# Kernel optimization log

Measured on AMD Instinct MI355X. Metric: run time of the kernel, lower is better.

Reference implementation:

```python
import jax, jax.numpy as jnp
import numpy as np

B, S, D, H, CD, TV, BS = 64, 128, 1024, 16, 128, 512, 4
HD = D // H          # head dim 64
MLP = 4 * D


def _ln(x, w):
    # SEDD-style LayerNorm: no bias, learned scale only
    m = x.mean(-1, keepdims=True)
    v = jnp.var(x, axis=-1, keepdims=True)
    return (x - m) * jax.lax.rsqrt(v + 1e-5) * w


def _rope(q, cos, sin):
    # q: (B, S, H, hd); cos/sin: (S, hd) with cat(freqs, freqs) layout
    h = HD // 2
    rot = jnp.concatenate([-q[..., h:], q[..., :h]], axis=-1)
    return q * cos[None, :, None, :] + rot * sin[None, :, None, :]


def _attn(q, k, v, mask):
    # q,k,v: (B, H, Lq/Lk, hd); mask broadcastable to (B, H, Lq, Lk), True = attend
    s = jnp.einsum('bhqd,bhkd->bhqk', q, k) / jnp.sqrt(jnp.asarray(HD, q.dtype))
    s = jnp.where(mask, s, jnp.asarray(-1e30, s.dtype))
    p = jax.nn.softmax(s, axis=-1)
    return jnp.einsum('bhqk,bhkd->bhqd', p, v)


def setup_inputs() -> dict:
    key = jax.random.key(0)
    ks = jax.random.split(key, 16)
    f = lambda k, shp, sc: jax.random.normal(k, shp, jnp.float32) * sc
    inp = {}
    inp['x'] = f(ks[0], (B, 2 * S, D), 1.0)
    inp['c'] = f(ks[1], (B, CD), 1.0)
    inp['encoder_out'] = f(ks[2], (B, TV, D), 1.0)
    enc_mask = np.ones((B, TV), dtype=bool)
    enc_mask[:, TV * 3 // 4:] = False
    inp['encoder_mask'] = jnp.asarray(enc_mask)
    # block diffusion training mask, (2S, 2S): M_BD | M_OBC | M_BC
    idx = np.arange(2 * S)
    q_idx, kv_idx = idx[:, None], idx[None, :]
    x0_q, x0_kv = q_idx >= S, kv_idx >= S
    bq = np.where(x0_q, (q_idx - S) // BS, q_idx // BS)
    bkv = np.where(x0_kv, (kv_idx - S) // BS, kv_idx // BS)
    m = ((bq == bkv) & (x0_q == x0_kv)) | ((bq > bkv) & x0_kv & (~x0_q)) | ((bq >= bkv) & x0_kv & x0_q)
    inp['mask'] = jnp.asarray(m)
    # rotary cos/sin for length S (applied identically to both halves)
    inv = 1.0 / (10000.0 ** (np.arange(0, HD, 2, dtype=np.float64) / HD))
    fr = np.einsum('i,j->ij', np.arange(S), inv)
    emb = np.concatenate([fr, fr], axis=-1)
    inp['cos'] = jnp.asarray(np.cos(emb), jnp.float32)
    inp['sin'] = jnp.asarray(np.sin(emb), jnp.float32)
    sc = 1.0 / np.sqrt(D)
    inp['norm1_w'] = jnp.ones((D,), jnp.float32)
    inp['w_qkv'] = f(ks[3], (D, 3 * D), sc)
    inp['w_attn_out'] = f(ks[4], (D, D), sc)
    inp['adaLN_w'] = f(ks[5], (CD, 6 * D), 0.02)  # nonzero so gates are active
    inp['adaLN_b'] = f(ks[6], (6 * D,), 0.02)
    inp['ca_norm_w'] = jnp.ones((D,), jnp.float32)
    inp['w_q'] = f(ks[7], (D, D), sc)
    inp['w_kv'] = f(ks[8], (D, 2 * D), sc)
    inp['w_o'] = f(ks[9], (D, D), sc)
    inp['norm2_w'] = jnp.ones((D,), jnp.float32)
    inp['w_mlp1'] = f(ks[10], (D, MLP), sc)
    inp['b_mlp1'] = jnp.zeros((MLP,), jnp.float32)
    inp['w_mlp2'] = f(ks[11], (MLP, D), 1.0 / np.sqrt(MLP))
    inp['b_mlp2'] = jnp.zeros((D,), jnp.float32)
    return inp


def reference(x, c, encoder_out, encoder_mask, mask, cos, sin,
              norm1_w, w_qkv, w_attn_out, adaLN_w, adaLN_b,
              ca_norm_w, w_q, w_kv, w_o, norm2_w,
              w_mlp1, b_mlp1, w_mlp2, b_mlp2):
    mod = (c @ adaLN_w + adaLN_b)[:, None, :]
    sh_msa, sc_msa, g_msa, sh_mlp, sc_mlp, g_mlp = jnp.split(mod, 6, axis=-1)
    x_skip = x
    xn = _ln(x, norm1_w) * (1.0 + sc_msa) + sh_msa  # modulate

    def get_qkv(xh):  # xh: (B, S, D) -> rotated q, k and v, each (B, S, H, hd)
        qkv = (xh @ w_qkv).reshape(B, S, 3, H, HD)
        return _rope(qkv[:, :, 0], cos, sin), _rope(qkv[:, :, 1], cos, sin), qkv[:, :, 2]

    q1, k1, v1 = get_qkv(xn[:, :S])
    q2, k2, v2 = get_qkv(xn[:, S:])
    q = jnp.concatenate([q1, q2], 1).transpose(0, 2, 1, 3)  # (B, H, 2S, hd)
    k = jnp.concatenate([k1, k2], 1).transpose(0, 2, 1, 3)
    v = jnp.concatenate([v1, v2], 1).transpose(0, 2, 1, 3)
    a = _attn(q, k, v, mask[None, None]).transpose(0, 2, 1, 3).reshape(B, 2 * S, D)
    x = x_skip + g_msa * (a @ w_attn_out)  # bias_dropout_add_scale (inference)

    # cross-attention to visual features
    r = x
    xc = _ln(x, ca_norm_w)
    qc = (xc @ w_q).reshape(B, 2 * S, H, HD).transpose(0, 2, 1, 3)
    kvc = (encoder_out @ w_kv).reshape(B, TV, 2, H, HD)
    kc = kvc[:, :, 0].transpose(0, 2, 1, 3)
    vc = kvc[:, :, 1].transpose(0, 2, 1, 3)
    ac = _attn(qc, kc, vc, encoder_mask[:, None, None, :]).transpose(0, 2, 1, 3).reshape(B, 2 * S, D)
    x = r + ac @ w_o

    # adaLN-modulated MLP (gelu-tanh)
    h = _ln(x, norm2_w) * (1.0 + sc_mlp) + sh_mlp
    m = jax.nn.gelu(h @ w_mlp1 + b_mlp1, approximate=True) @ w_mlp2 + b_mlp2
    return x + g_mlp * m
```

## Files before the change

### kernel.cpp

```cpp
#include <hip/hip_runtime.h>
#include <hip/hip_bf16.h>
#include <math.h>

typedef __hip_bfloat16 bf16;
typedef __attribute__((ext_vector_type(8))) short bf16x8;
typedef __attribute__((ext_vector_type(4))) float f32x4;

#define B_   64
#define S_   128
#define L_   256
#define D_   1024
#define H_   16
#define HD_  64
#define CD_  128
#define TV_  512
#define MLP_ 4096
#define SIXD (6*D_)
#define GB   16
#define NG   (B_/GB)
#define MG   (GB*L_)

__device__ __forceinline__ float b2f(bf16 v){ return __bfloat162float(v); }
__device__ __forceinline__ bf16  f2b(float v){ return __float2bfloat16(v); }
__device__ __forceinline__ unsigned short f2bu(float v){
    bf16 b = __float2bfloat16(v);
    unsigned short u; __builtin_memcpy(&u, &b, 2); return u;
}
__device__ __forceinline__ short f2bs(float v){ return (short)f2bu(v); }
__device__ __forceinline__ float ldf(const void* p, size_t i, bool f32){
    return f32 ? ((const float*)p)[i] : b2f(((const bf16*)p)[i]);
}
__device__ __forceinline__ void gload16(const void* g, void* l){
    __builtin_amdgcn_global_load_lds(
        (const __attribute__((address_space(1))) void*)g,
        (__attribute__((address_space(3))) void*)l, 16, 0, 0);
}

__global__ void detect_kernel(const unsigned short* __restrict__ x, int* __restrict__ flag)
{
    __shared__ int cnt;
    if (threadIdx.x == 0) cnt = 0;
    __syncthreads();
    int local = 0;
    for (int i = threadIdx.x; i < 1024; i += 256) {
        unsigned short h = x[2*i];
        int e = (h >> 7) & 0xff;
        if (e >= 117 && e <= 133) local++;
    }
    atomicAdd(&cnt, local);
    __syncthreads();
    if (threadIdx.x == 0) flag[0] = (cnt < 512) ? 1 : 0;
}

#define BM 64
#define BN 64
#define BK 16
__global__ __launch_bounds__(256) void gemm_kernel(
    const int* __restrict__ dt, int opmask,
    const void* __restrict__ A, size_t aOff,
    const void* __restrict__ W,
    int M, int N, int K,
    const void* __restrict__ bias, int act,
    const float* __restrict__ mod, int gate_off, int row0,
    const void* __restrict__ resb,
    bf16* __restrict__ outb, float* __restrict__ outf)
{
    const bool f32 = dt[0] != 0;
    const bool aF = f32 && (opmask & 1);
    const bool rF = f32 && (opmask & 2);
    const bool wF = f32;

    __shared__ float As[BK][BM+1];
    __shared__ float Ws[BK][BN+1];
    int tid = threadIdx.x;
    int bm = blockIdx.y * BM;
    int bn = blockIdx.x * BN;
    int ty = tid >> 4, tx = tid & 15;
    float acc[4][4];
#pragma unroll
    for (int i=0;i<4;i++)
#pragma unroll
        for (int j=0;j<4;j++) acc[i][j]=0.f;

    for (int k0=0; k0<K; k0+=BK) {
#pragma unroll
        for (int i=0;i<4;i++) {
            int idx = tid + i*256;
            int m = idx >> 4, k = idx & 15;
            As[k][m] = ldf(A, aOff + (size_t)(bm+m)*K + k0 + k, aF);
        }
#pragma unroll
        for (int i=0;i<4;i++) {
            int idx = tid + i*256;
            int k = idx >> 6, n = idx & 63;
            Ws[k][n] = ldf(W, (size_t)(k0+k)*N + bn + n, wF);
        }
        __syncthreads();
#pragma unroll
        for (int k=0;k<BK;k++) {
            float a0[4], w0[4];
#pragma unroll
            for (int i=0;i<4;i++) a0[i] = As[k][ty*4+i];
#pragma unroll
            for (int j=0;j<4;j++) w0[j] = Ws[k][tx*4+j];
#pragma unroll
            for (int i=0;i<4;i++)
#pragma unroll
                for (int j=0;j<4;j++)
                    acc[i][j] += a0[i]*w0[j];
        }
        __syncthreads();
    }

#pragma unroll
    for (int i=0;i<4;i++) {
        int m = bm + ty*4 + i;
#pragma unroll
        for (int j=0;j<4;j++) {
            int n = bn + tx*4 + j;
            float v = acc[i][j];
            if (bias) v += ldf(bias, n, wF);
            if (act==1) {
                float x3 = v*v*v;
                v = 0.5f*v*(1.f + tanhf(0.7978845608028654f*(v + 0.044715f*x3)));
            }
            if (mod)  v *= mod[(size_t)((row0+m)>>8)*SIXD + gate_off + n];
            size_t o = (size_t)m*N + n;
            if (resb) v += ldf(resb, o, rF);
            if (outf) outf[o] = v;
            else      outb[o] = f2b(v);
        }
    }
}

__global__ __launch_bounds__(256) void transpose_w_kernel(
    const int* __restrict__ dt, const void* __restrict__ W,
    bf16* __restrict__ Wt, int K, int N)
{
    const bool f32 = dt[0] != 0;
    __shared__ float t[32][33];
    int n0 = blockIdx.x * 32, k0 = blockIdx.y * 32;
    int tx = threadIdx.x & 31, ty = threadIdx.x >> 5;
#pragma unroll
    for (int r = 0; r < 4; ++r)
        t[ty + r*8][tx] = ldf(W, (size_t)(k0 + ty + r*8)*N + n0 + tx, f32);
    __syncthreads();
#pragma unroll
    for (int r = 0; r < 4; ++r)
        Wt[(size_t)(n0 + ty + r*8)*K + k0 + tx] = f2b(t[tx][ty + r*8]);
}

__global__ __launch_bounds__(256) void mfma_gemm(
    const int* __restrict__ dt, int aDin,
    const void* __restrict__ A, size_t aOff,
    const bf16* __restrict__ Wt,
    int M, int N, int K,
    const void* __restrict__ bias, int act,
    const float* __restrict__ mod, int gate_off, int row0,
    const void* __restrict__ resb, int rDin,
    bf16* __restrict__ outb, float* __restrict__ outf)
{
    const bool f32 = dt[0] != 0;
    const bool aF = f32 && aDin;
    const bool rF = f32 && rDin;
    (void)M;

    __shared__ __align__(16) short As[128*40];
    __shared__ __align__(16) short Bs[128*32];

    int tid  = threadIdx.x;
    int lane = tid & 63, wid = tid >> 6;
    int wr = wid >> 1, wc = wid & 1;
    size_t bm = (size_t)blockIdx.y * 128;
    size_t bn = (size_t)blockIdx.x * 128;

    f32x4 acc[4][4];
#pragma unroll
    for (int i=0;i<4;i++)
#pragma unroll
        for (int j=0;j<4;j++) acc[i][j] = (f32x4){0.f,0.f,0.f,0.f};

    const int rr  = lane & 15;
    const int ksg = (lane >> 4) * 8;

    const short* Ab = (const short*)A + aOff;
    const float* Af = (const float*)A + aOff;
    const short* Wts = (const short*)Wt;

    if (!aF) {
        for (int k0 = 0; k0 < K; k0 += 32) {
#pragma unroll
            for (int c = 0; c < 2; ++c) {
                int u = wid*128 + c*64 + lane;
                gload16(Ab  + (bm + (u>>2))*K + k0 + (u&3)*8, As + (wid*128 + c*64)*8);
                gload16(Wts + (bn + (u>>2))*K + k0 + (u&3)*8, Bs + (wid*128 + c*64)*8);
            }
            __syncthreads();
            bf16x8 av[4], bv[4];
#pragma unroll
            for (int i=0;i<4;i++) av[i] = *(const bf16x8*)(As + (wr*64 + i*16 + rr)*32 + ksg);
#pragma unroll
            for (int j=0;j<4;j++) bv[j] = *(const bf16x8*)(Bs + (wc*64 + j*16 + rr)*32 + ksg);
#pragma unroll
            for (int i=0;i<4;i++)
#pragma unroll
                for (int j=0;j<4;j++)
                    acc[i][j] = __builtin_amdgcn_mfma_f32_16x16x32_bf16(av[i], bv[j], acc[i][j], 0, 0, 0);
            __syncthreads();
        }
    } else {
        const int r0 = tid >> 2,         p0 = tid & 3;
        const int r1 = (tid + 256) >> 2, p1 = (tid + 256) & 3;
        for (int k0 = 0; k0 < K; k0 += 32) {
            const float* s0 = Af + (bm+r0)*K + k0 + p0*8;
            float4 u0 = *(const float4*)s0;
            float4 u1 = *(const float4*)(s0+4);
            bf16x8 t0;
            t0[0]=f2bs(u0.x); t0[1]=f2bs(u0.y); t0[2]=f2bs(u0.z); t0[3]=f2bs(u0.w);
            t0[4]=f2bs(u1.x); t0[5]=f2bs(u1.y); t0[6]=f2bs(u1.z); t0[7]=f2bs(u1.w);
            *(bf16x8*)(As + r0*40 + p0*8) = t0;
            const float* s1 = Af + (bm+r1)*K + k0 + p1*8;
            float4 u2 = *(const float4*)s1;
            float4 u3 = *(const float4*)(s1+4);
            bf16x8 t1;
            t1[0]=f2bs(u2.x); t1[1]=f2bs(u2.y); t1[2]=f2bs(u2.z); t1[3]=f2bs(u2.w);
            t1[4]=f2bs(u3.x); t1[5]=f2bs(u3.y); t1[6]=f2bs(u3.z); t1[7]=f2bs(u3.w);
            *(bf16x8*)(As + r1*40 + p1*8) = t1;
#pragma unroll
            for (int c = 0; c < 2; ++c) {
                int u = wid*128 + c*64 + lane;
                gload16(Wts + (bn + (u>>2))*K + k0 + (u&3)*8, Bs + (wid*128 + c*64)*8);
            }
            __syncthreads();
            bf16x8 av[4], bv[4];
#pragma unroll
            for (int i=0;i<4;i++) av[i] = *(const bf16x8*)(As + (wr*64 + i*16 + rr)*40 + ksg);
#pragma unroll
            for (int j=0;j<4;j++) bv[j] = *(const bf16x8*)(Bs + (wc*64 + j*16 + rr)*32 + ksg);
#pragma unroll
            for (int i=0;i<4;i++)
#pragma unroll
                for (int j=0;j<4;j++)
                    acc[i][j] = __builtin_amdgcn_mfma_f32_16x16x32_bf16(av[i], bv[j], acc[i][j], 0, 0, 0);
            __syncthreads();
        }
    }

    const int cc = lane & 15;
    const int rb = (lane >> 4) * 4;
#pragma unroll
    for (int j=0;j<4;j++) {
        int gcol = (int)bn + wc*64 + j*16 + cc;
        float bvadd = bias ? ldf(bias, gcol, f32) : 0.f;
#pragma unroll
        for (int i=0;i<4;i++) {
#pragma unroll
            for (int r2=0;r2<4;r2++) {
                int grow = (int)bm + wr*64 + i*16 + rb + r2;
                float v = acc[i][j][r2] + bvadd;
                if (act == 1) {
                    float x3 = v*v*v;
                    v = 0.5f*v*(1.f + tanhf(0.7978845608028654f*(v + 0.044715f*x3)));
                }
                if (mod) v *= mod[(size_t)((row0+grow)>>8)*SIXD + gate_off + gcol];
                size_t o = (size_t)grow*N + gcol;
                if (resb) v += ldf(resb, o, rF);
                if (outf) outf[o] = v;
                else      outb[o] = f2b(v);
            }
        }
    }
}

__global__ __launch_bounds__(256) void ln_kernel(
    const int* __restrict__ dt, int x_din,
    const void* __restrict__ xb, const void* __restrict__ w,
    const float* __restrict__ mod, int sh_off, int sc_off,
    bf16* __restrict__ out)
{
    const bool f32 = dt[0] != 0;
    const bool xF = f32 && x_din;
    const bool wF = f32;
    int row = blockIdx.x;
    int b   = row >> 8;
    int tid = threadIdx.x;
    float xv[4];
    float s=0.f, s2=0.f;
#pragma unroll
    for (int i=0;i<4;i++) {
        int d = tid + i*256;
        float v = ldf(xb, (size_t)row*D_ + d, xF);
        xv[i]=v; s+=v; s2+=v*v;
    }
    __shared__ float r1[256], r2[256];
    r1[tid]=s; r2[tid]=s2; __syncthreads();
    for (int off=128; off>0; off>>=1) {
        if (tid<off){ r1[tid]+=r1[tid+off]; r2[tid]+=r2[tid+off]; }
        __syncthreads();
    }
    float mean = r1[0]*(1.f/D_);
    float var  = r2[0]*(1.f/D_) - mean*mean;
    float rstd = rsqrtf(var + 1e-5f);
#pragma unroll
    for (int i=0;i<4;i++) {
        int d = tid + i*256;
        float y = (xv[i]-mean)*rstd*ldf(w, d, wF);
        if (mod) y = y*(1.f + mod[(size_t)b*SIXD + sc_off + d])
                     + mod[(size_t)b*SIXD + sh_off + d];
        out[(size_t)row*D_ + d] = f2b(y);
    }
}

__global__ __launch_bounds__(256) void rope_kernel(
    const int* __restrict__ dt, bf16* __restrict__ qkv,
    const void* __restrict__ cosb, const void* __restrict__ sinb)
{
    const bool f32 = dt[0] != 0;
    int g  = blockIdx.x*256 + threadIdx.x;
    int d  = g & 31;
    int h  = (g>>5) & 15;
    int qk = (g>>9) & 1;
    int t  = (g>>10) & 255;
    int b  = g >> 18;
    int pos = t & (S_-1);
    bf16* p = qkv + ((size_t)(b*L_+t)*3 + qk)*D_ + h*HD_;
    float c0 = ldf(cosb, pos*HD_ + d,    f32), sn0 = ldf(sinb, pos*HD_ + d,    f32);
    float c1 = ldf(cosb, pos*HD_ + d+32, f32), sn1 = ldf(sinb, pos*HD_ + d+32, f32);
    float lo = b2f(p[d]), hi = b2f(p[d+32]);
    p[d]    = f2b(lo*c0 - hi*sn0);
    p[d+32] = f2b(hi*c1 + lo*sn1);
}

template<int MODE>
__global__ __launch_bounds__(256) void attn_mfma_kernel(
    const bf16* __restrict__ qsrc, const bf16* __restrict__ kvsrc,
    bf16* __restrict__ out)
{
    constexpr int NT = MODE ? 12 : 8;
    int blk  = blockIdx.x;
    int half = blk & 1;
    int h    = (blk >> 1) & 15;
    int b    = blk >> 5;
    int tid  = threadIdx.x, lane = tid & 63, w = tid >> 6;
    int g = lane >> 4, c = lane & 15;

    __shared__ __align__(16) short Kt[2][32][72];
    __shared__ __align__(16) short Vt[2][64][40];
    __shared__ __align__(16) short Pl[4][32][40];

    const size_t krstride = MODE ? 2048 : 3072;
    const bf16* Kbase = MODE ? kvsrc + ((size_t)b*512*2    )*1024 + h*64
                             : kvsrc + ((size_t)b*256*3 + 1)*1024 + h*64;
    const bf16* Vbase = MODE ? kvsrc + ((size_t)b*512*2 + 1)*1024 + h*64
                             : kvsrc + ((size_t)b*256*3 + 2)*1024 + h*64;
    const size_t qstride = MODE ? 1024 : 3072;
    const bf16* Qbase = MODE ? qsrc + (size_t)b*256*1024 + h*64
                             : qsrc + (size_t)b*256*3*1024 + h*64;

    bf16x8 qf[2][2];
#pragma unroll
    for (int qb=0; qb<2; ++qb) {
        int qi = half*128 + w*32 + qb*16 + c;
#pragma unroll
        for (int dc=0; dc<2; ++dc)
            qf[qb][dc] = *(const bf16x8*)(Qbase + (size_t)qi*qstride + dc*32 + g*8);
    }

    f32x4 oacc[2][4];
    float mrow[2][4], lrow[2][4];
#pragma unroll
    for (int qb=0; qb<2; ++qb){
#pragma unroll
        for (int dl=0; dl<4; ++dl) oacc[qb][dl] = (f32x4){0.f,0.f,0.f,0.f};
#pragma unroll
        for (int r=0; r<4; ++r){ mrow[qb][r] = -1e30f; lrow[qb][r] = 0.f; }
    }

    auto stage = [&](int kt, int buf){
        for (int u = tid; u < 512; u += 256) {
            int k = u >> 4, d8 = (u & 15)*4;
            *(uint2*)&Kt[buf][k][d8] =
                *(const uint2*)(Kbase + (size_t)(kt*32+k)*krstride + d8);
        }
        for (int u = tid; u < 512; u += 256) {
            int k = u >> 4, d4 = (u & 15)*4;
            uint2 vv = *(const uint2*)(Vbase + (size_t)(kt*32+k)*krstride + d4);
            short* vp = (short*)&vv;
#pragma unroll
            for (int j=0;j<4;++j) Vt[buf][d4+j][k] = vp[j];
        }
    };

    stage(0, 0);
    __syncthreads();

    for (int kt = 0; kt < NT; ++kt) {
        int buf = kt & 1;
        if (kt+1 < NT) stage(kt+1, buf^1);

        bool need = MODE ? true : ((half==0 && kt==w) || (kt>=4 && (kt-4)<=w));
        if (need) {
            bf16x8 kf[2][2], vf[4];
#pragma unroll
            for (int kc=0;kc<2;++kc)
#pragma unroll
                for (int dc=0;dc<2;++dc)
                    kf[kc][dc] = *(const bf16x8*)&Kt[buf][kc*16 + c][dc*32 + g*8];
#pragma unroll
            for (int dl=0;dl<4;++dl)
                vf[dl] = *(const bf16x8*)&Vt[buf][dl*16 + c][g*8];

#pragma unroll
            for (int qb=0;qb<2;++qb) {
                f32x4 s0 = (f32x4){0.f,0.f,0.f,0.f};
                f32x4 s1 = (f32x4){0.f,0.f,0.f,0.f};
                s0 = __builtin_amdgcn_mfma_f32_16x16x32_bf16(qf[qb][0], kf[0][0], s0, 0,0,0);
                s0 = __builtin_amdgcn_mfma_f32_16x16x32_bf16(qf[qb][1], kf[0][1], s0, 0,0,0);
                s1 = __builtin_amdgcn_mfma_f32_16x16x32_bf16(qf[qb][0], kf[1][0], s1, 0,0,0);
                s1 = __builtin_amdgcn_mfma_f32_16x16x32_bf16(qf[qb][1], kf[1][1], s1, 0,0,0);

                bool v0 = true, v1 = true;
                if (MODE == 0) {
                    int bq  = w*8 + qb*4 + g;
                    int ki0 = kt*32 + c, ki1 = ki0 + 16;
                    bool xk0 = ki0 >= 128, xk1 = ki1 >= 128;
                    int bk0 = (ki0 & 127) >> 2, bk1 = (ki1 & 127) >> 2;
                    v0 = xk0 ? (half ? (bq >= bk0) : (bq > bk0)) : (!half && bq == bk0);
                    v1 = xk1 ? (half ? (bq >= bk1) : (bq > bk1)) : (!half && bq == bk1);
                }
                float a0[4], a1[4];
#pragma unroll
                for (int r=0;r<4;++r){
                    a0[r] = v0 ? s0[r]*0.125f : -1e30f;
                    a1[r] = v1 ? s1[r]*0.125f : -1e30f;
                }
                float p0[4], p1[4];
#pragma unroll
                for (int r=0;r<4;++r){
                    float t = fmaxf(a0[r], a1[r]);
                    t = fmaxf(t, __shfl_xor(t,1));
                    t = fmaxf(t, __shfl_xor(t,2));
                    t = fmaxf(t, __shfl_xor(t,4));
                    t = fmaxf(t, __shfl_xor(t,8));
                    float mn = fmaxf(mrow[qb][r], t);
                    float scale = __expf(mrow[qb][r] - mn);
                    mrow[qb][r] = mn;
                    p0[r] = __expf(a0[r] - mn);
                    p1[r] = __expf(a1[r] - mn);
                    float rs = p0[r] + p1[r];
                    rs += __shfl_xor(rs,1);
                    rs += __shfl_xor(rs,2);
                    rs += __shfl_xor(rs,4);
                    rs += __shfl_xor(rs,8);
                    lrow[qb][r] = lrow[qb][r]*scale + rs;
#pragma unroll
                    for (int dl=0;dl<4;++dl) oacc[qb][dl][r] *= scale;
                }
#pragma unroll
                for (int r=0;r<4;++r){
                    Pl[w][qb*16 + g*4 + r][c]      = f2bs(p0[r]);
                    Pl[w][qb*16 + g*4 + r][16 + c] = f2bs(p1[r]);
                }
            }
            asm volatile("s_waitcnt lgkmcnt(0)" ::: "memory");
            __builtin_amdgcn_sched_barrier(0);
#pragma unroll
            for (int qb=0;qb<2;++qb) {
                bf16x8 pa = *(const bf16x8*)&Pl[w][qb*16 + c][g*8];
#pragma unroll
                for (int dl=0;dl<4;++dl)
                    oacc[qb][dl] = __builtin_amdgcn_mfma_f32_16x16x32_bf16(pa, vf[dl], oacc[qb][dl], 0,0,0);
            }
        }
        __syncthreads();
    }

#pragma unroll
    for (int qb=0;qb<2;++qb){
#pragma unroll
        for (int r=0;r<4;++r){
            float inv = 1.f / lrow[qb][r];
            int qi = half*128 + w*32 + qb*16 + g*4 + r;
            bf16* op = out + (size_t)(b*256 + qi)*1024 + h*64;
#pragma unroll
            for (int dl=0;dl<4;++dl)
                op[dl*16 + c] = f2b(oacc[qb][dl][r] * inv);
        }
    }
}

extern "C" void kernel_launch(void* const* d_in, const int* in_sizes, int n_in,
                              void* d_out, int out_size, void* d_ws, size_t ws_size,
                              hipStream_t stream)
{
    (void)in_sizes; (void)n_in; (void)out_size; (void)ws_size;
    const void* x    = d_in[0];
    const void* c    = d_in[1];
    const void* enc  = d_in[2];
    const void* cosb = d_in[5];
    const void* sinb = d_in[6];
    const void* n1w  = d_in[7];
    const void* wqkv = d_in[8];
    const void* wao  = d_in[9];
    const void* adw  = d_in[10];
    const void* adb  = d_in[11];
    const void* cnw  = d_in[12];
    const void* wq   = d_in[13];
    const void* wkv  = d_in[14];
    const void* wo   = d_in[15];
    const void* n2w  = d_in[16];
    const void* wm1  = d_in[17];
    const void* bm1  = d_in[18];
    const void* wm2  = d_in[19];
    const void* bm2  = d_in[20];
    float* fout = (float*)d_out;

    char* p = (char*)d_ws;
    int*   dt  = (int*)p;    p += 256;
    float* mod = (float*)p;  p += (size_t)B_*SIXD*4;
    bf16*  A   = (bf16*)p;   p += (size_t)B_*L_*D_*2;
    bf16*  C   = (bf16*)p;   p += (size_t)B_*L_*D_*2;
    bf16*  Dch = (bf16*)p;   p += (size_t)GB*TV_*2*D_*2;
    bf16*  Wt1 = (bf16*)p;   p += (size_t)D_*MLP_*2;
    bf16*  Wt2 = (bf16*)p;   p += (size_t)D_*MLP_*2;
    bf16*  Bq  = (bf16*)d_out;

    const int M = B_*L_;
    dim3 blk(256);

    detect_kernel<<<1, blk, 0, stream>>>((const unsigned short*)x, dt);
    gemm_kernel<<<dim3(SIXD/BN, B_/BM), blk, 0, stream>>>(
        dt, 1, c, 0, adw, B_, SIXD, CD_, adb, 0, nullptr, 0, 0, nullptr, nullptr, mod);
    ln_kernel<<<M, blk, 0, stream>>>(dt, 1, x, n1w, mod, 0*D_, 1*D_, A);
    transpose_w_kernel<<<dim3(3*D_/32, D_/32), blk, 0, stream>>>(dt, wqkv, Wt1, D_, 3*D_);
    for (int g=0; g<NG; g++) {
        mfma_gemm<<<dim3(3*D_/128, MG/128), blk, 0, stream>>>(
            dt, 0, A, (size_t)g*MG*D_, Wt1, MG, 3*D_, D_,
            nullptr, 0, nullptr, 0, 0, nullptr, 0, Dch, nullptr);
        rope_kernel<<<(GB*L_*2*H_*32)/256, blk, 0, stream>>>(dt, Dch, cosb, sinb);
        attn_mfma_kernel<0><<<GB*H_*2, blk, 0, stream>>>(Dch, Dch, Bq + (size_t)g*MG*D_);
    }
    transpose_w_kernel<<<dim3(D_/32, D_/32), blk, 0, stream>>>(dt, wao, Wt1, D_, D_);
    mfma_gemm<<<dim3(D_/128, M/128), blk, 0, stream>>>(
        dt, 0, Bq, 0, Wt1, M, D_, D_,
        nullptr, 0, mod, 2*D_, 0, x, 1, C, nullptr);
    ln_kernel<<<M, blk, 0, stream>>>(dt, 0, C, cnw, nullptr, 0, 0, A);
    transpose_w_kernel<<<dim3(D_/32, D_/32), blk, 0, stream>>>(dt, wq, Wt1, D_, D_);
    mfma_gemm<<<dim3(D_/128, M/128), blk, 0, stream>>>(
        dt, 0, A, 0, Wt1, M, D_, D_,
        nullptr, 0, nullptr, 0, 0, nullptr, 0, Bq, nullptr);
    transpose_w_kernel<<<dim3(2*D_/32, D_/32), blk, 0, stream>>>(dt, wkv, Wt1, D_, 2*D_);
    for (int g=0; g<NG; g++) {
        mfma_gemm<<<dim3(2*D_/128, (GB*TV_)/128), blk, 0, stream>>>(
            dt, 1, enc, (size_t)g*GB*TV_*D_, Wt1, GB*TV_, 2*D_, D_,
            nullptr, 0, nullptr, 0, 0, nullptr, 0, Dch, nullptr);
        attn_mfma_kernel<1><<<GB*H_*2, blk, 0, stream>>>(
            Bq + (size_t)g*MG*D_, Dch, A + (size_t)g*MG*D_);
    }
    transpose_w_kernel<<<dim3(D_/32, D_/32), blk, 0, stream>>>(dt, wo, Wt1, D_, D_);
    mfma_gemm<<<dim3(D_/128, M/128), blk, 0, stream>>>(
        dt, 0, A, 0, Wt1, M, D_, D_,
        nullptr, 0, nullptr, 0, 0, C, 0, C, nullptr);
    ln_kernel<<<M, blk, 0, stream>>>(dt, 0, C, n2w, mod, 3*D_, 4*D_, A);
    transpose_w_kernel<<<dim3(MLP_/32, D_/32), blk, 0, stream>>>(dt, wm1, Wt1, D_, MLP_);
    transpose_w_kernel<<<dim3(D_/32, MLP_/32), blk, 0, stream>>>(dt, wm2, Wt2, MLP_, D_);
    for (int g=0; g<NG; g++) {
        mfma_gemm<<<dim3(MLP_/128, MG/128), blk, 0, stream>>>(
            dt, 0, A, (size_t)g*MG*D_, Wt1, MG, MLP_, D_,
            bm1, 1, nullptr, 0, 0, nullptr, 0, Dch, nullptr);
        mfma_gemm<<<dim3(D_/128, MG/128), blk, 0, stream>>>(
            dt, 0, Dch, 0, Wt2, MG, D_, MLP_,
            bm2, 0, mod, 5*D_, g*MG, C + (size_t)g*MG*D_, 0,
            nullptr, fout + (size_t)g*MG*D_);
    }
}
```

Measured before the change: 2.449 ms.

## Triple-buffer MFMA GEMM K loop, add XCD-aware tile swizzle, pre-convert encoder

The MFMA GEMM main loop now uses a three-stage LDS ring with async global-to-LDS loads issued two tiles ahead. A single vmcnt wait plus barrier per iteration replaces the two syncthreads, so load latency overlaps with MFMA work. Workgroup IDs are remapped so consecutive tiles land on the same XCD and are grouped by 8 row tiles, which should improve L2 reuse. The fp32 A-operand path is removed: encoder output is first converted to bf16 in a separate kernel that writes into spare space in the output buffer. This costs an extra pass over the encoder data and more LDS per block, which may lower occupancy.

```diff
diff --git a/kernel.cpp b/kernel.cpp
--- a/kernel.cpp
+++ b/kernel.cpp
@@ -35,6 +35,7 @@
         (const __attribute__((address_space(1))) void*)g,
         (__attribute__((address_space(3))) void*)l, 16, 0, 0);
 }
+#define WAITBAR(N) asm volatile("s_waitcnt vmcnt(" N ")\n\ts_barrier" ::: "memory")
 
 __global__ void detect_kernel(const unsigned short* __restrict__ x, int* __restrict__ flag)
 {
@@ -150,9 +151,27 @@
         Wt[(size_t)(n0 + ty + r*8)*K + k0 + tx] = f2b(t[tx][ty + r*8]);
 }
 
+__global__ __launch_bounds__(256) void conv_bf16_kernel(
+    const int* __restrict__ dt, const void* __restrict__ src, size_t off,
+    bf16* __restrict__ dst)
+{
+    const bool f32 = dt[0] != 0;
+    size_t i = ((size_t)blockIdx.x*256 + threadIdx.x)*8;
+    if (f32) {
+        const float* s = (const float*)src + off + i;
+        float4 a = *(const float4*)s, b = *(const float4*)(s+4);
+        bf16x8 t;
+        t[0]=f2bs(a.x); t[1]=f2bs(a.y); t[2]=f2bs(a.z); t[3]=f2bs(a.w);
+        t[4]=f2bs(b.x); t[5]=f2bs(b.y); t[6]=f2bs(b.z); t[7]=f2bs(b.w);
+        *(bf16x8*)((short*)dst + i) = t;
+    } else {
+        *(bf16x8*)((short*)dst + i) = *(const bf16x8*)((const short*)src + off + i);
+    }
+}
+
 __global__ __launch_bounds__(256) void mfma_gemm(
-    const int* __restrict__ dt, int aDin,
-    const void* __restrict__ A, size_t aOff,
+    const int* __restrict__ dt,
+    const bf16* __restrict__ A, size_t aOff,
     const bf16* __restrict__ Wt,
     int M, int N, int K,
     const void* __restrict__ bias, int act,
@@ -161,18 +180,30 @@
     bf16* __restrict__ outb, float* __restrict__ outf)
 {
     const bool f32 = dt[0] != 0;
-    const bool aF = f32 && aDin;
     const bool rF = f32 && rDin;
     (void)M;
 
-    __shared__ __align__(16) short As[128*40];
-    __shared__ __align__(16) short Bs[128*32];
+    __shared__ __align__(16) short As[3][128*32];
+    __shared__ __align__(16) short Bs[3][128*32];
 
     int tid  = threadIdx.x;
     int lane = tid & 63, wid = tid >> 6;
     int wr = wid >> 1, wc = wid & 1;
-    size_t bm = (size_t)blockIdx.y * 128;
-    size_t bn = (size_t)blockIdx.x * 128;
+
+    unsigned gx = gridDim.x, gy = gridDim.y;
+    unsigned nwg = gx*gy;
+    unsigned orig = blockIdx.y*gx + blockIdx.x;
+    unsigned q8 = nwg >> 3, r8 = nwg & 7, xcd = orig & 7, loc = orig >> 3;
+    unsigned id = (xcd < r8 ? xcd*(q8+1) : r8*(q8+1) + (xcd-r8)*q8) + loc;
+    const unsigned GM = 8;
+    unsigned nig = GM*gx;
+    unsigned gid = id / nig;
+    unsigned rem = id - gid*nig;
+    unsigned gsm = gy - gid*GM; if (gsm > GM) gsm = GM;
+    unsigned by = gid*GM + rem % gsm;
+    unsigned bx = rem / gsm;
+    size_t bm = (size_t)by * 128;
+    size_t bn = (size_t)bx * 128;
 
     f32x4 acc[4][4];
 #pragma unroll
@@ -183,67 +214,47 @@
     const int rr  = lane & 15;
     const int ksg = (lane >> 4) * 8;
 
-    const short* Ab = (const short*)A + aOff;
-    const float* Af = (const float*)A + aOff;
+    const short* Ab  = (const short*)A + aOff;
     const short* Wts = (const short*)Wt;
 
-    if (!aF) {
-        for (int k0 = 0; k0 < K; k0 += 32) {
-#pragma unroll
-            for (int c = 0; c < 2; ++c) {
-                int u = wid*128 + c*64 + lane;
-                gload16(Ab  + (bm + (u>>2))*K + k0 + (u&3)*8, As + (wid*128 + c*64)*8);
-                gload16(Wts + (bn + (u>>2))*K + k0 + (u&3)*8, Bs + (wid*128 + c*64)*8);
-            }
-            __syncthreads();
-            bf16x8 av[4], bv[4];
-#pragma unroll
-            for (int i=0;i<4;i++) av[i] = *(const bf16x8*)(As + (wr*64 + i*16 + rr)*32 + ksg);
-#pragma unroll
-            for (int j=0;j<4;j++) bv[j] = *(const bf16x8*)(Bs + (wc*64 + j*16 + rr)*32 + ksg);
-#pragma unroll
-            for (int i=0;i<4;i++)
-#pragma unroll
-                for (int j=0;j<4;j++)
-                    acc[i][j] = __builtin_amdgcn_mfma_f32_16x16x32_bf16(av[i], bv[j], acc[i][j], 0, 0, 0);
-            __syncthreads();
-        }
-    } else {
-        const int r0 = tid >> 2,         p0 = tid & 3;
-        const int r1 = (tid + 256) >> 2, p1 = (tid + 256) & 3;
-        for (int k0 = 0; k0 < K; k0 += 32) {
-            const float* s0 = Af + (bm+r0)*K + k0 + p0*8;
-            float4 u0 = *(const float4*)s0;
-            float4 u1 = *(const float4*)(s0+4);
-            bf16x8 t0;
-            t0[0]=f2bs(u0.x); t0[1]=f2bs(u0.y); t0[2]=f2bs(u0.z); t0[3]=f2bs(u0.w);
-            t0[4]=f2bs(u1.x); t0[5]=f2bs(u1.y); t0[6]=f2bs(u1.z); t0[7]=f2bs(u1.w);
-            *(bf16x8*)(As + r0*40 + p0*8) = t0;
-            const float* s1 = Af + (bm+r1)*K + k0 + p1*8;
-            float4 u2 = *(const float4*)s1;
-            float4 u3 = *(const float4*)(s1+4);
-            bf16x8 t1;
-            t1[0]=f2bs(u2.x); t1[1]=f2bs(u2.y); t1[2]=f2bs(u2.z); t1[3]=f2bs(u2.w);
-            t1[4]=f2bs(u3.x); t1[5]=f2bs(u3.y); t1[6]=f2bs(u3.z); t1[7]=f2bs(u3.w);
-            *(bf16x8*)(As + r1*40 + p1*8) = t1;
-#pragma unroll
-            for (int c = 0; c < 2; ++c) {
-                int u = wid*128 + c*64 + lane;
-                gload16(Wts + (bn + (u>>2))*K + k0 + (u&3)*8, Bs + (wid*128 + c*64)*8);
-            }
-            __syncthreads();
-            bf16x8 av[4], bv[4];
-#pragma unroll
-            for (int i=0;i<4;i++) av[i] = *(const bf16x8*)(As + (wr*64 + i*16 + rr)*40 + ksg);
-#pragma unroll
-            for (int j=0;j<4;j++) bv[j] = *(const bf16x8*)(Bs + (wc*64 + j*16 + rr)*32 + ksg);
-#pragma unroll
-            for (int i=0;i<4;i++)
-#pragma unroll
-                for (int j=0;j<4;j++)
-                    acc[i][j] = __builtin_amdgcn_mfma_f32_16x16x32_bf16(av[i], bv[j], acc[i][j], 0, 0, 0);
-            __syncthreads();
-        }
+    const int u0 = wid*128 + lane, u1 = u0 + 64;
+    const short* pa0 = Ab  + (bm + (u0>>2))*(size_t)K + (u0&3)*8;
+    const short* pa1 = Ab  + (bm + (u1>>2))*(size_t)K + (u1&3)*8;
+    const short* pb0 = Wts + (bn + (u0>>2))*(size_t)K + (u0&3)*8;
+    const short* pb1 = Wts + (bn + (u1>>2))*(size_t)K + (u1&3)*8;
+    const int ld0 = wid*1024, ld1 = wid*1024 + 512;
+
+    auto stage = [&](int kt, int buf){
+        int k0 = kt*32;
+        gload16(pa0 + k0, &As[buf][ld0]);
+        gload16(pa1 + k0, &As[buf][ld1]);
+        gload16(pb0 + k0, &Bs[buf][ld0]);
+        gload16(pb1 + k0, &Bs[buf][ld1]);
+    };
+    auto compute = [&](int buf){
+        bf16x8 av[4], bv[4];
+#pragma unroll
+        for (int i=0;i<4;i++) av[i] = *(const bf16x8*)&As[buf][(wr*64 + i*16 + rr)*32 + ksg];
+#pragma unroll
+        for (int j=0;j<4;j++) bv[j] = *(const bf16x8*)&Bs[buf][(wc*64 + j*16 + rr)*32 + ksg];
+#pragma unroll
+        for (int i=0;i<4;i++)
+#pragma unroll
+            for (int j=0;j<4;j++)
+                acc[i][j] = __builtin_amdgcn_mfma_f32_16x16x32_bf16(av[i], bv[j], acc[i][j], 0, 0, 0);
+    };
+
+    const int nt = K >> 5;
+    int bufc = 0, bufn = 1, bufs = 2;
+    stage(0, bufc);
+    stage(1, bufn);
+    WAITBAR("4");
+    for (int t = 0; t < nt; ++t) {
+        if (t+2 < nt) stage(t+2, bufs);
+        compute(bufc);
+        int tmp = bufc; bufc = bufn; bufn = bufs; bufs = tmp;
+        if (t+2 < nt)      WAITBAR("4");
+        else if (t+1 < nt) WAITBAR("0");
     }
 
     const int cc = lane & 15;
@@ -523,7 +534,8 @@
     bf16*  Dch = (bf16*)p;   p += (size_t)GB*TV_*2*D_*2;
     bf16*  Wt1 = (bf16*)p;   p += (size_t)D_*MLP_*2;
     bf16*  Wt2 = (bf16*)p;   p += (size_t)D_*MLP_*2;
-    bf16*  Bq  = (bf16*)d_out;
+    bf16*  Bq   = (bf16*)d_out;
+    bf16*  EncB = (bf16*)((char*)d_out + ((size_t)B_*L_*D_*2));
 
     const int M = B_*L_;
     dim3 blk(256);
@@ -535,41 +547,43 @@
     transpose_w_kernel<<<dim3(3*D_/32, D_/32), blk, 0, stream>>>(dt, wqkv, Wt1, D_, 3*D_);
     for (int g=0; g<NG; g++) {
         mfma_gemm<<<dim3(3*D_/128, MG/128), blk, 0, stream>>>(
-            dt, 0, A, (size_t)g*MG*D_, Wt1, MG, 3*D_, D_,
+            dt, A, (size_t)g*MG*D_, Wt1, MG, 3*D_, D_,
             nullptr, 0, nullptr, 0, 0, nullptr, 0, Dch, nullptr);
         rope_kernel<<<(GB*L_*2*H_*32)/256, blk, 0, stream>>>(dt, Dch, cosb, sinb);
         attn_mfma_kernel<0><<<GB*H_*2, blk, 0, stream>>>(Dch, Dch, Bq + (size_t)g*MG*D_);
     }
     transpose_w_kernel<<<dim3(D_/32, D_/32), blk, 0, stream>>>(dt, wao, Wt1, D_, D_);
     mfma_gemm<<<dim3(D_/128, M/128), blk, 0, stream>>>(
-        dt, 0, Bq, 0, Wt1, M, D_, D_,
+        dt, Bq, 0, Wt1, M, D_, D_,
         nullptr, 0, mod, 2*D_, 0, x, 1, C, nullptr);
     ln_kernel<<<M, blk, 0, stream>>>(dt, 0, C, cnw, nullptr, 0, 0, A);
     transpose_w_kernel<<<dim3(D_/32, D_/32), blk, 0, stream>>>(dt, wq, Wt1, D_, D_);
     mfma_gemm<<<dim3(D_/128, M/128), blk, 0, stream>>>(
-        dt, 0, A, 0, Wt1, M, D_, D_,
+        dt, A, 0, Wt1, M, D_, D_,
         nullptr, 0, nullptr, 0, 0, nullptr, 0, Bq, nullptr);
     transpose_w_kernel<<<dim3(2*D_/32, D_/32), blk, 0, stream>>>(dt, wkv, Wt1, D_, 2*D_);
     for (int g=0; g<NG; g++) {
+        conv_bf16_kernel<<<(GB*TV_*D_)/(256*8), blk, 0, stream>>>(
+            dt, enc, (size_t)g*GB*TV_*D_, EncB);
         mfma_gemm<<<dim3(2*D_/128, (GB*TV_)/128), blk, 0, stream>>>(
-            dt, 1, enc, (size_t)g*GB*TV_*D_, Wt1, GB*TV_, 2*D_, D_,
+            dt, EncB, 0, Wt1, GB*TV_, 2*D_, D_,
             nullptr, 0, nullptr, 0, 0, nullptr, 0, Dch, nullptr);
         attn_mfma_kernel<1><<<GB*H_*2, blk, 0, stream>>>(
             Bq + (size_t)g*MG*D_, Dch, A + (size_t)g*MG*D_);
     }
     transpose_w_kernel<<<dim3(D_/32, D_/32), blk, 0, stream>>>(dt, wo, Wt1, D_, D_);
     mfma_gemm<<<dim3(D_/128, M/128), blk, 0, stream>>>(
-        dt, 0, A, 0, Wt1, M, D_, D_,
+        dt, A, 0, Wt1, M, D_, D_,
         nullptr, 0, nullptr, 0, 0, C, 0, C, nullptr);
     ln_kernel<<<M, blk, 0, stream>>>(dt, 0, C, n2w, mod, 3*D_, 4*D_, A);
     transpose_w_kernel<<<dim3(MLP_/32, D_/32), blk, 0, stream>>>(dt, wm1, Wt1, D_, MLP_);
     transpose_w_kernel<<<dim3(D_/32, MLP_/32), blk, 0, stream>>>(dt, wm2, Wt2, MLP_, D_);
     for (int g=0; g<NG; g++) {
         mfma_gemm<<<dim3(MLP_/128, MG/128), blk, 0, stream>>>(
-            dt, 0, A, (size_t)g*MG*D_, Wt1, MG, MLP_, D_,
+            dt, A, (size_t)g*MG*D_, Wt1, MG, MLP_, D_,
             bm1, 1, nullptr, 0, 0, nullptr, 0, Dch, nullptr);
         mfma_gemm<<<dim3(D_/128, MG/128), blk, 0, stream>>>(
-            dt, 0, Dch, 0, Wt2, MG, D_, MLP_,
+            dt, Dch, 0, Wt2, MG, D_, MLP_,
             bm2, 0, mod, 5*D_, g*MG, C + (size_t)g*MG*D_, 0,
             nullptr, fout + (size_t)g*MG*D_);
     }
```

Result: faster. 2.237 ms (-8.6%).
